# Kernel tuning notes

Hardware: AMD Instinct MI355X
Metric: run time of the kernel (lower is better)

## Reference

```python
import jax, jax.numpy as jnp
import numpy as np
import math

NH, NKV, D = 32, 8, 128  # heads, kv heads, head dim

def _alibi_slopes(n):
    cp2 = 2 ** math.floor(math.log2(n))
    base = 2.0 ** (-8.0 / cp2)
    slopes = base ** np.arange(1, cp2 + 1, dtype=np.float32)
    if cp2 != n:
        extra_base = 2.0 ** (-4.0 / cp2)
        extra = extra_base ** np.arange(1, 1 + 2 * (n - cp2), 2, dtype=np.float32)
        slopes = np.concatenate([slopes, extra])
    return slopes.astype(np.float32)

def setup_inputs() -> dict:
    key = jax.random.key(0)
    k1, k2, k3 = jax.random.split(key, 3)
    B, S, H = 4, 1024, 4096
    qkv_out = NH * D + 2 * NKV * D  # 6144
    return {
        "hidden_states": jax.random.normal(k1, (B, S, H), jnp.float32) * 0.02,
        "w_qkv": jax.random.normal(k2, (H, qkv_out), jnp.float32) * 0.02,
        "w_o": jax.random.normal(k3, (NH * D, H), jnp.float32) * 0.02,
    }

def reference(hidden_states, w_qkv, w_o):
    B, S, H = hidden_states.shape
    G = NH // NKV  # query groups per kv head
    scale = D ** -0.5

    qkv = hidden_states @ w_qkv  # [B,S,6144]
    q = qkv[..., : NH * D].reshape(B, S, NKV, G, D)
    k = qkv[..., NH * D : NH * D + NKV * D].reshape(B, S, NKV, D)
    v = qkv[..., NH * D + NKV * D :].reshape(B, S, NKV, D)

    scores = jnp.einsum("bqhgd,bkhd->bhgqk", q, k) * scale  # [B,NKV,G,S,S]

    slopes = jnp.asarray(_alibi_slopes(NH)).reshape(NKV, G)  # head order
    pos = jnp.arange(S)
    rel = pos[:, None] - pos[None, :]  # i - j
    sqrt_dist = jnp.sqrt(jnp.maximum(rel, 0).astype(jnp.float32))
    bias = -slopes[:, :, None, None] * sqrt_dist  # ALiBi-sqrt bias
    bias = jnp.where(rel[None, None] >= 0, bias, -jnp.inf)  # causal mask

    attn = jax.nn.softmax(scores + bias[None], axis=-1)
    out = jnp.einsum("bhgqk,bkhd->bqhgd", attn, v).reshape(B, S, NH * D)
    return out @ w_o
```

## Files before the change

kernel.cpp:

```cpp
#include <hip/hip_runtime.h>
#include <stdint.h>

typedef __attribute__((ext_vector_type(4))) float floatx4;
typedef __attribute__((ext_vector_type(8))) short short8;
typedef unsigned short ushort_t;

#define DEVI __device__ __forceinline__

constexpr int Bc   = 4;
constexpr int Sc   = 1024;
constexpr int Hc   = 4096;
constexpr int NHc  = 32;
constexpr int NKVc = 8;
constexpr int Dc   = 128;
constexpr int QKVO = 6144;
constexpr int Mc   = Bc * Sc;

DEVI ushort_t f2bf(float f) {
  union { float f; unsigned u; } x; x.f = f;
  unsigned u = x.u;
  u += 0x7fffu + ((u >> 16) & 1u);
  return (ushort_t)(u >> 16);
}

DEVI short8 cvt8(floatx4 a, floatx4 b) {
  short8 r;
  r[0] = (short)f2bf(a[0]); r[1] = (short)f2bf(a[1]);
  r[2] = (short)f2bf(a[2]); r[3] = (short)f2bf(a[3]);
  r[4] = (short)f2bf(b[0]); r[5] = (short)f2bf(b[1]);
  r[6] = (short)f2bf(b[2]); r[7] = (short)f2bf(b[3]);
  return r;
}

DEVI void load_lds16(const ushort_t* g, ushort_t* l) {
  __builtin_amdgcn_global_load_lds(
      (const __attribute__((address_space(1))) void*)g,
      (__attribute__((address_space(3))) void*)l, 16, 0, 0);
}

#define BARRIER()  asm volatile("s_barrier" ::: "memory")
#define VMCNT(n)   asm volatile("s_waitcnt vmcnt(" #n ")" ::: "memory")

__global__ __launch_bounds__(256)
void cvt_bf16(const float* __restrict__ src, ushort_t* __restrict__ dst, int n8)
{
  const int i = blockIdx.x * 256 + threadIdx.x;
  if (i >= n8) return;
  const floatx4 f0 = *(const floatx4*)(src + (size_t)i * 8);
  const floatx4 f1 = *(const floatx4*)(src + (size_t)i * 8 + 4);
  *(short8*)(dst + (size_t)i * 8) = cvt8(f0, f1);
}

__global__ __launch_bounds__(256)
void transpose_cvt(const float* __restrict__ src, ushort_t* __restrict__ dst,
                   int R, int C)
{
  __shared__ float ts[64][67];
  const int cb = C >> 6;
  const int r0 = (blockIdx.x / cb) << 6;
  const int c0 = (blockIdx.x % cb) << 6;
  const int t  = threadIdx.x;

  const int lr = t >> 4, lc = (t & 15) << 2;
#pragma unroll
  for (int i = 0; i < 4; ++i) {
    const floatx4 v = *(const floatx4*)(src + (size_t)(r0 + lr + 16 * i) * C + c0 + lc);
#pragma unroll
    for (int j = 0; j < 4; ++j) ts[lr + 16 * i][lc + j] = v[j];
  }
  __syncthreads();

  const int c     = ((t >> 6) << 4) + ((t & 63) >> 2);
  const int chunk = t & 3;
  short8 t0, t1;
#pragma unroll
  for (int k = 0; k < 8; ++k) t0[k] = (short)f2bf(ts[chunk * 16 + k][c]);
#pragma unroll
  for (int k = 0; k < 8; ++k) t1[k] = (short)f2bf(ts[chunk * 16 + 8 + k][c]);
  ushort_t* dp = dst + (size_t)(c0 + c) * R + r0 + chunk * 16;
  *(short8*)dp       = t0;
  *(short8*)(dp + 8) = t1;
}

__global__ __launch_bounds__(256)
void v_transpose(const ushort_t* __restrict__ qkv, ushort_t* __restrict__ vt)
{
  __shared__ ushort_t ts[64][72];
  const int bid = blockIdx.x;
  const int db  = bid & 1;
  const int sb  = (bid >> 1) & 15;
  const int hkv = (bid >> 5) & 7;
  const int b   = bid >> 8;
  const int t   = threadIdx.x;

  const ushort_t* src = qkv + (size_t)(b * Sc + sb * 64) * QKVO
                        + (NHc * Dc + NKVc * Dc) + hkv * Dc + db * 64;
  const int lr = t >> 3, lc = (t & 7) * 8;
  *(short8*)&ts[lr][lc]      = *(const short8*)(src + (size_t)lr * QKVO + lc);
  *(short8*)&ts[lr + 32][lc] = *(const short8*)(src + (size_t)(lr + 32) * QKVO + lc);
  __syncthreads();

  ushort_t* dst = vt + ((size_t)(b * NKVc + hkv) * Dc + db * 64) * Sc + sb * 64;
  const int dr  = t >> 2;
  const int sc0 = (t & 3) * 16;
  short8 o0, o1;
#pragma unroll
  for (int k = 0; k < 8; ++k) o0[k] = (short)ts[sc0 + k][dr];
#pragma unroll
  for (int k = 0; k < 8; ++k) o1[k] = (short)ts[sc0 + 8 + k][dr];
  *(short8*)(dst + (size_t)dr * Sc + sc0)     = o0;
  *(short8*)(dst + (size_t)dr * Sc + sc0 + 8) = o1;
}

template<bool OBF16>
__global__ __launch_bounds__(512, 2)
void gemm_nt8(const ushort_t* __restrict__ A, const ushort_t* __restrict__ BT,
              void* __restrict__ Cp, int M, int N, int K)
{
  __shared__ __align__(16) ushort_t As[2][256 * 64];
  __shared__ __align__(16) ushort_t Bs[2][256 * 64];

  const int nb  = N >> 8;
  const int nwg = (M >> 8) * nb;
  int bid = blockIdx.x;
  bid = (bid & 7) * (nwg >> 3) + (bid >> 3);
  const int bm = bid / nb, bn = bid % nb;
  const int m0 = bm << 8, n0 = bn << 8;

  const int tid  = threadIdx.x;
  const int wid  = tid >> 6, lane = tid & 63;
  const int wm   = wid >> 2, wn = wid & 3;
  const int fr   = lane & 15;
  const int g16  = (lane >> 4) << 4;
  const int rsw  = (fr & 7) << 4;
  const int l8   = lane >> 3;
  const int scol = ((lane & 7) ^ l8) << 3;

  const int abase = ((wid >> 2) << 7) + ((wid & 3) << 4);
  const int bbase = wid << 5;

  const size_t Ks = (size_t)K;
  const ushort_t* ag = A  + (size_t)(m0 + abase + l8) * K + scol;
  const ushort_t* bg = BT + (size_t)(n0 + bbase + l8) * K + scol;

  const int rowA = (wm * 128 + fr) * 128;
  const int rowB = (wn * 64 + fr) * 128;
  const int cb0  = g16 ^ rsw;
  const int cb1  = (64 + g16) ^ rsw;

  const floatx4 fz = {0.f, 0.f, 0.f, 0.f};
  floatx4 acc[8][4];
#pragma unroll
  for (int i = 0; i < 8; ++i)
#pragma unroll
    for (int f = 0; f < 4; ++f) acc[i][f] = fz;

  auto STAGE = [&](int v, size_t kn) {
    load_lds16(ag + kn,            &As[v][(abase +  0) * 64]);
    load_lds16(ag +  8 * Ks + kn,  &As[v][(abase +  8) * 64]);
    load_lds16(bg + kn,            &Bs[v][(bbase +  0) * 64]);
    load_lds16(bg +  8 * Ks + kn,  &Bs[v][(bbase +  8) * 64]);
    load_lds16(ag + 64 * Ks + kn,  &As[v][(abase + 64) * 64]);
    load_lds16(ag + 72 * Ks + kn,  &As[v][(abase + 72) * 64]);
    load_lds16(bg + 16 * Ks + kn,  &Bs[v][(bbase + 16) * 64]);
    load_lds16(bg + 24 * Ks + kn,  &Bs[v][(bbase + 24) * 64]);
  };

  STAGE(0, 0);
  VMCNT(4);
  BARRIER();

  const int NT = K >> 6;
  for (int kt = 0; kt < NT; ++kt) {
    const int u = kt & 1, v = u ^ 1;
    const char* Au = (const char*)&As[u][0];
    const char* Bu = (const char*)&Bs[u][0];
    const bool st  = (kt + 1 < NT);

#define LDA(i, ks) (*(const short8*)(Au + rowA + (i) * 2048 + ((ks) ? cb1 : cb0)))
#define LDB(f, ks) (*(const short8*)(Bu + rowB + (f) * 2048 + ((ks) ? cb1 : cb0)))
#define MFMA16(d, a0, a1, b0, b1)                                         \
    d = __builtin_amdgcn_mfma_f32_16x16x32_bf16(a0, b0, d, 0, 0, 0);      \
    d = __builtin_amdgcn_mfma_f32_16x16x32_bf16(a1, b1, d, 0, 0, 0);

    short8 aL[4][2], aH[4][2], bE[2][2], bO[2][2];

#pragma unroll
    for (int i = 0; i < 4; ++i) { aL[i][0] = LDA(i, 0); aL[i][1] = LDA(i, 1); }
#pragma unroll
    for (int f = 0; f < 2; ++f) { bE[f][0] = LDB(2 * f, 0); bE[f][1] = LDB(2 * f, 1); }
    if (st) STAGE(v, (size_t)(kt + 1) << 6);
    BARRIER();
    __builtin_amdgcn_s_setprio(1);
#pragma unroll
    for (int i = 0; i < 4; ++i)
#pragma unroll
      for (int f = 0; f < 2; ++f) { MFMA16(acc[i][2 * f], aL[i][0], aL[i][1], bE[f][0], bE[f][1]); }
    __builtin_amdgcn_s_setprio(0);
    if (st) { VMCNT(10); } else { VMCNT(2); }
    BARRIER();

#pragma unroll
    for (int i = 0; i < 4; ++i) { aH[i][0] = LDA(4 + i, 0); aH[i][1] = LDA(4 + i, 1); }
    BARRIER();
    __builtin_amdgcn_s_setprio(1);
#pragma unroll
    for (int i = 0; i < 4; ++i)
#pragma unroll
      for (int f = 0; f < 2; ++f) { MFMA16(acc[4 + i][2 * f], aH[i][0], aH[i][1], bE[f][0], bE[f][1]); }
    __builtin_amdgcn_s_setprio(0);
    if (st) { VMCNT(8); } else { VMCNT(0); }
    BARRIER();

#pragma unroll
    for (int f = 0; f < 2; ++f) { bO[f][0] = LDB(2 * f + 1, 0); bO[f][1] = LDB(2 * f + 1, 1); }
    BARRIER();
    __builtin_amdgcn_s_setprio(1);
#pragma unroll
    for (int i = 0; i < 4; ++i)
#pragma unroll
      for (int f = 0; f < 2; ++f) { MFMA16(acc[4 + i][2 * f + 1], aH[i][0], aH[i][1], bO[f][0], bO[f][1]); }
    __builtin_amdgcn_s_setprio(0);
    BARRIER();

    __builtin_amdgcn_s_setprio(1);
#pragma unroll
    for (int i = 0; i < 4; ++i)
#pragma unroll
      for (int f = 0; f < 2; ++f) { MFMA16(acc[i][2 * f + 1], aL[i][0], aL[i][1], bO[f][0], bO[f][1]); }
    __builtin_amdgcn_s_setprio(0);
    if (st) { VMCNT(4); }
    BARRIER();

#undef LDA
#undef LDB
#undef MFMA16
  }

  const int r4 = (lane >> 4) << 2;
#pragma unroll
  for (int i = 0; i < 8; ++i) {
#pragma unroll
    for (int rr = 0; rr < 4; ++rr) {
      const size_t row = (size_t)(m0 + wm * 128 + i * 16 + r4 + rr);
#pragma unroll
      for (int f = 0; f < 4; ++f) {
        const size_t col = (size_t)(n0 + wn * 64 + f * 16 + fr);
        if constexpr (OBF16)
          ((ushort_t*)Cp)[row * N + col] = f2bf(acc[i][f][rr]);
        else
          ((float*)Cp)[row * N + col] = acc[i][f][rr];
      }
    }
  }
}

__global__ __launch_bounds__(256, 2)
void attn_fwd(const ushort_t* __restrict__ qkv,
              const ushort_t* __restrict__ vt,
              ushort_t* __restrict__ attn)
{
  __shared__ __align__(16) ushort_t Plds[4][32 * 40];

  const int bid = blockIdx.x;
  const int x   = bid & 7;
  const int p   = bid >> 3;
  const int j   = p & 15;
  const int g   = ((p >> 4) << 3) + x;
  const int b   = g >> 3;
  const int hkv = g & 7;

  const int tid  = threadIdx.x;
  const int wid  = tid >> 6, lane = tid & 63;
  const int h    = hkv * 4 + wid;
  const int fr   = lane & 15;
  const int kk8  = (lane >> 4) << 3;
  const int q4   = (lane >> 4) << 2;
  const float slope = exp2f(-0.25f * (float)(h + 1));
  const float scale = 0.08838834764831845f;

  const ushort_t* qp  = qkv + (size_t)b * Sc * QKVO + (size_t)h * Dc;
  const ushort_t* kp  = qkv + (size_t)b * Sc * QKVO + NHc * Dc + (size_t)hkv * Dc;
  const ushort_t* vtp = vt + (size_t)(b * NKVc + hkv) * Dc * Sc;
  ushort_t* myP = &Plds[wid][0];

  const floatx4 fz = {0.f, 0.f, 0.f, 0.f};

  auto process = [&](const int qb) {
    short8 qf[2][4];
#pragma unroll
    for (int t = 0; t < 2; ++t) {
      const int qrow = qb * 32 + t * 16 + fr;
#pragma unroll
      for (int s = 0; s < 4; ++s)
        qf[t][s] = *(const short8*)(qp + (size_t)qrow * QKVO + s * 32 + kk8);
    }

    floatx4 o[2][8];
#pragma unroll
    for (int t = 0; t < 2; ++t)
#pragma unroll
      for (int jj = 0; jj < 8; ++jj) o[t][jj] = fz;
    float mrow[2][4], lrow[2][4];
#pragma unroll
    for (int t = 0; t < 2; ++t)
#pragma unroll
      for (int rr = 0; rr < 4; ++rr) { mrow[t][rr] = -1e30f; lrow[t][rr] = 0.f; }

    for (int kb = 0; kb <= qb; ++kb) {
      floatx4 s_[2][2];
      s_[0][0] = fz; s_[0][1] = fz; s_[1][0] = fz; s_[1][1] = fz;
#pragma unroll
      for (int half = 0; half < 2; ++half) {
        const int kcol = kb * 32 + half * 16 + fr;
#pragma unroll
        for (int s = 0; s < 4; ++s) {
          const short8 kf = *(const short8*)(kp + (size_t)kcol * QKVO + s * 32 + kk8);
          s_[0][half] = __builtin_amdgcn_mfma_f32_16x16x32_bf16(qf[0][s], kf, s_[0][half], 0, 0, 0);
          s_[1][half] = __builtin_amdgcn_mfma_f32_16x16x32_bf16(qf[1][s], kf, s_[1][half], 0, 0, 0);
        }
      }

      short8 vf[8];
#pragma unroll
      for (int jj = 0; jj < 8; ++jj)
        vf[jj] = *(const short8*)(vtp + (size_t)(jj * 16 + fr) * Sc + kb * 32 + kk8);

#pragma unroll
      for (int t = 0; t < 2; ++t)
#pragma unroll
        for (int rr = 0; rr < 4; ++rr) {
          const int qg  = qb * 32 + t * 16 + q4 + rr;
          const int dk0 = qg - (kb * 32 + fr);
          const int dk1 = dk0 - 16;
          s_[t][0][rr] = (dk0 >= 0)
              ? s_[t][0][rr] * scale - slope * sqrtf((float)dk0) : -1e30f;
          s_[t][1][rr] = (dk1 >= 0)
              ? s_[t][1][rr] * scale - slope * sqrtf((float)dk1) : -1e30f;
        }

      float pmv[2][4];
#pragma unroll
      for (int t = 0; t < 2; ++t)
#pragma unroll
        for (int rr = 0; rr < 4; ++rr) {
          float pm = fmaxf(s_[t][0][rr], s_[t][1][rr]);
#pragma unroll
          for (int m = 1; m < 16; m <<= 1) pm = fmaxf(pm, __shfl_xor(pm, m));
          pmv[t][rr] = pm;
        }

      int need = 0;
#pragma unroll
      for (int t = 0; t < 2; ++t)
#pragma unroll
        for (int rr = 0; rr < 4; ++rr)
          need |= (pmv[t][rr] > mrow[t][rr] + 8.f) ? 1 : 0;
      if (__any(need)) {
#pragma unroll
        for (int t = 0; t < 2; ++t)
#pragma unroll
          for (int rr = 0; rr < 4; ++rr) {
            const float mnew = fmaxf(mrow[t][rr], pmv[t][rr]);
            const float corr = __expf(mrow[t][rr] - mnew);
            lrow[t][rr] *= corr;
            mrow[t][rr] = mnew;
#pragma unroll
            for (int jj = 0; jj < 8; ++jj) o[t][jj][rr] *= corr;
          }
      }

#pragma unroll
      for (int t = 0; t < 2; ++t)
#pragma unroll
        for (int rr = 0; rr < 4; ++rr) {
          const float p0 = __expf(s_[t][0][rr] - mrow[t][rr]);
          const float p1 = __expf(s_[t][1][rr] - mrow[t][rr]);
          lrow[t][rr] += p0 + p1;
          myP[(t * 16 + q4 + rr) * 40 + fr]      = f2bf(p0);
          myP[(t * 16 + q4 + rr) * 40 + 16 + fr] = f2bf(p1);
        }
      short8 pa[2];
      pa[0] = *(const short8*)&myP[fr * 40 + kk8];
      pa[1] = *(const short8*)&myP[(16 + fr) * 40 + kk8];

#pragma unroll
      for (int jj = 0; jj < 8; ++jj) {
        o[0][jj] = __builtin_amdgcn_mfma_f32_16x16x32_bf16(pa[0], vf[jj], o[0][jj], 0, 0, 0);
        o[1][jj] = __builtin_amdgcn_mfma_f32_16x16x32_bf16(pa[1], vf[jj], o[1][jj], 0, 0, 0);
      }
    }

#pragma unroll
    for (int t = 0; t < 2; ++t)
#pragma unroll
      for (int rr = 0; rr < 4; ++rr) {
        float rs = lrow[t][rr];
#pragma unroll
        for (int m = 1; m < 16; m <<= 1) rs += __shfl_xor(rs, m);
        const float inv = 1.f / rs;
        const size_t tok = (size_t)b * Sc + qb * 32 + t * 16 + q4 + rr;
#pragma unroll
        for (int jj = 0; jj < 8; ++jj)
          attn[tok * (size_t)(NHc * Dc) + h * Dc + jj * 16 + fr] = f2bf(o[t][jj][rr] * inv);
      }
  };

  process(31 - j);
  process(j);
}

extern "C" void kernel_launch(void* const* d_in, const int* in_sizes, int n_in,
                              void* d_out, int out_size, void* d_ws, size_t ws_size,
                              hipStream_t stream)
{
  const float* hidden = (const float*)d_in[0];
  const float* w_qkv  = (const float*)d_in[1];
  const float* w_o    = (const float*)d_in[2];
  float* out = (float*)d_out;

  ushort_t* wqT   = (ushort_t*)d_ws;
  ushort_t* hidb  = wqT + (size_t)QKVO * Hc;
  ushort_t* qkvb  = hidb + (size_t)Mc * Hc;
  ushort_t* attnb = hidb;
  ushort_t* woT   = wqT;
  ushort_t* vtb   = wqT + (size_t)Mc * Hc;

  cvt_bf16<<<dim3((Mc * Hc / 8) / 256), dim3(256), 0, stream>>>(
      hidden, hidb, Mc * Hc / 8);
  transpose_cvt<<<dim3((Hc / 64) * (QKVO / 64)), dim3(256), 0, stream>>>(
      w_qkv, wqT, Hc, QKVO);
  gemm_nt8<true><<<dim3((Mc / 256) * (QKVO / 256)), dim3(512), 0, stream>>>(
      hidb, wqT, qkvb, Mc, QKVO, Hc);
  v_transpose<<<dim3(1024), dim3(256), 0, stream>>>(qkvb, vtb);
  attn_fwd<<<dim3(512), dim3(256), 0, stream>>>(qkvb, vtb, attnb);
  transpose_cvt<<<dim3((Hc / 64) * (Hc / 64)), dim3(256), 0, stream>>>(
      w_o, woT, Hc, Hc);
  gemm_nt8<false><<<dim3((Mc / 256) * (Hc / 256)), dim3(512), 0, stream>>>(
      attnb, woT, out, Mc, Hc, Hc);
}
```

Before: 578.9 us.

## Restructure GEMM main loop into K-half phases with split A/B staging

Result: slower. 599.1 us (+3.5%).

```diff
diff --git a/kernel.cpp b/kernel.cpp
--- a/kernel.cpp
+++ b/kernel.cpp
@@ -39,6 +39,7 @@
 }
 
 #define BARRIER()  asm volatile("s_barrier" ::: "memory")
+#define LGKM0()    asm volatile("s_waitcnt lgkmcnt(0)" ::: "memory")
 #define VMCNT(n)   asm volatile("s_waitcnt vmcnt(" #n ")" ::: "memory")
 
 __global__ __launch_bounds__(256)
@@ -136,12 +137,10 @@
   const int l8   = lane >> 3;
   const int scol = ((lane & 7) ^ l8) << 3;
 
-  const int abase = ((wid >> 2) << 7) + ((wid & 3) << 4);
-  const int bbase = wid << 5;
-
+  const int sr   = (wid << 3);
   const size_t Ks = (size_t)K;
-  const ushort_t* ag = A  + (size_t)(m0 + abase + l8) * K + scol;
-  const ushort_t* bg = BT + (size_t)(n0 + bbase + l8) * K + scol;
+  const ushort_t* agS = A  + (size_t)(m0 + sr + l8) * K + scol;
+  const ushort_t* bgS = BT + (size_t)(n0 + sr + l8) * K + scol;
 
   const int rowA = (wm * 128 + fr) * 128;
   const int rowB = (wn * 64 + fr) * 128;
@@ -155,19 +154,21 @@
 #pragma unroll
     for (int f = 0; f < 4; ++f) acc[i][f] = fz;
 
-  auto STAGE = [&](int v, size_t kn) {
-    load_lds16(ag + kn,            &As[v][(abase +  0) * 64]);
-    load_lds16(ag +  8 * Ks + kn,  &As[v][(abase +  8) * 64]);
-    load_lds16(bg + kn,            &Bs[v][(bbase +  0) * 64]);
-    load_lds16(bg +  8 * Ks + kn,  &Bs[v][(bbase +  8) * 64]);
-    load_lds16(ag + 64 * Ks + kn,  &As[v][(abase + 64) * 64]);
-    load_lds16(ag + 72 * Ks + kn,  &As[v][(abase + 72) * 64]);
-    load_lds16(bg + 16 * Ks + kn,  &Bs[v][(bbase + 16) * 64]);
-    load_lds16(bg + 24 * Ks + kn,  &Bs[v][(bbase + 24) * 64]);
+  auto STB = [&](int v, size_t kn) {
+    load_lds16(bgS + kn,            &Bs[v][(sr +   0) * 64]);
+    load_lds16(bgS +  64 * Ks + kn, &Bs[v][(sr +  64) * 64]);
+    load_lds16(bgS + 128 * Ks + kn, &Bs[v][(sr + 128) * 64]);
+    load_lds16(bgS + 192 * Ks + kn, &Bs[v][(sr + 192) * 64]);
   };
-
-  STAGE(0, 0);
-  VMCNT(4);
+  auto STA = [&](int v, size_t kn) {
+    load_lds16(agS + kn,            &As[v][(sr +   0) * 64]);
+    load_lds16(agS + 128 * Ks + kn, &As[v][(sr + 128) * 64]);
+    load_lds16(agS +  64 * Ks + kn, &As[v][(sr +  64) * 64]);
+    load_lds16(agS + 192 * Ks + kn, &As[v][(sr + 192) * 64]);
+  };
+
+  STB(0, 0); STA(0, 0);
+  VMCNT(2);
   BARRIER();
 
   const int NT = K >> 6;
@@ -176,65 +177,74 @@
     const char* Au = (const char*)&As[u][0];
     const char* Bu = (const char*)&Bs[u][0];
     const bool st  = (kt + 1 < NT);
+    const size_t kn = (size_t)(kt + 1) << 6;
 
 #define LDA(i, ks) (*(const short8*)(Au + rowA + (i) * 2048 + ((ks) ? cb1 : cb0)))
 #define LDB(f, ks) (*(const short8*)(Bu + rowB + (f) * 2048 + ((ks) ? cb1 : cb0)))
-#define MFMA16(d, a0, a1, b0, b1)                                         \
-    d = __builtin_amdgcn_mfma_f32_16x16x32_bf16(a0, b0, d, 0, 0, 0);      \
-    d = __builtin_amdgcn_mfma_f32_16x16x32_bf16(a1, b1, d, 0, 0, 0);
-
-    short8 aL[4][2], aH[4][2], bE[2][2], bO[2][2];
-
-#pragma unroll
-    for (int i = 0; i < 4; ++i) { aL[i][0] = LDA(i, 0); aL[i][1] = LDA(i, 1); }
-#pragma unroll
-    for (int f = 0; f < 2; ++f) { bE[f][0] = LDB(2 * f, 0); bE[f][1] = LDB(2 * f, 1); }
-    if (st) STAGE(v, (size_t)(kt + 1) << 6);
-    BARRIER();
+
+    short8 aR[4], bR[4];
+
+#pragma unroll
+    for (int i = 0; i < 4; ++i) aR[i] = LDA(i, 0);
+#pragma unroll
+    for (int f = 0; f < 4; ++f) bR[f] = LDB(f, 0);
+    if (st) { STB(v, kn); VMCNT(4); } else { VMCNT(0); }
+    BARRIER();
+    LGKM0(); __builtin_amdgcn_sched_barrier(0);
     __builtin_amdgcn_s_setprio(1);
 #pragma unroll
     for (int i = 0; i < 4; ++i)
 #pragma unroll
-      for (int f = 0; f < 2; ++f) { MFMA16(acc[i][2 * f], aL[i][0], aL[i][1], bE[f][0], bE[f][1]); }
+      for (int f = 0; f < 4; ++f)
+        acc[i][f] = __builtin_amdgcn_mfma_f32_16x16x32_bf16(aR[i], bR[f], acc[i][f], 0, 0, 0);
     __builtin_amdgcn_s_setprio(0);
-    if (st) { VMCNT(10); } else { VMCNT(2); }
-    BARRIER();
-
-#pragma unroll
-    for (int i = 0; i < 4; ++i) { aH[i][0] = LDA(4 + i, 0); aH[i][1] = LDA(4 + i, 1); }
-    BARRIER();
+    BARRIER();
+
+#pragma unroll
+    for (int i = 0; i < 4; ++i) aR[i] = LDA(4 + i, 0);
+    if (st) STA(v, kn);
+    BARRIER();
+    LGKM0(); __builtin_amdgcn_sched_barrier(0);
     __builtin_amdgcn_s_setprio(1);
 #pragma unroll
     for (int i = 0; i < 4; ++i)
 #pragma unroll
-      for (int f = 0; f < 2; ++f) { MFMA16(acc[4 + i][2 * f], aH[i][0], aH[i][1], bE[f][0], bE[f][1]); }
+      for (int f = 0; f < 4; ++f)
+        acc[4 + i][f] = __builtin_amdgcn_mfma_f32_16x16x32_bf16(aR[i], bR[f], acc[4 + i][f], 0, 0, 0);
     __builtin_amdgcn_s_setprio(0);
-    if (st) { VMCNT(8); } else { VMCNT(0); }
-    BARRIER();
-
-#pragma unroll
-    for (int f = 0; f < 2; ++f) { bO[f][0] = LDB(2 * f + 1, 0); bO[f][1] = LDB(2 * f + 1, 1); }
-    BARRIER();
+    BARRIER();
+
+#pragma unroll
+    for (int i = 0; i < 4; ++i) aR[i] = LDA(4 + i, 1);
+#pragma unroll
+    for (int f = 0; f < 4; ++f) bR[f] = LDB(f, 1);
+    BARRIER();
+    LGKM0(); __builtin_amdgcn_sched_barrier(0);
     __builtin_amdgcn_s_setprio(1);
 #pragma unroll
     for (int i = 0; i < 4; ++i)
 #pragma unroll
-      for (int f = 0; f < 2; ++f) { MFMA16(acc[4 + i][2 * f + 1], aH[i][0], aH[i][1], bO[f][0], bO[f][1]); }
+      for (int f = 0; f < 4; ++f)
+        acc[4 + i][f] = __builtin_amdgcn_mfma_f32_16x16x32_bf16(aR[i], bR[f], acc[4 + i][f], 0, 0, 0);
     __builtin_amdgcn_s_setprio(0);
     BARRIER();
 
+#pragma unroll
+    for (int i = 0; i < 4; ++i) aR[i] = LDA(i, 1);
+    if (st) { VMCNT(2); }
+    BARRIER();
+    LGKM0(); __builtin_amdgcn_sched_barrier(0);
     __builtin_amdgcn_s_setprio(1);
 #pragma unroll
     for (int i = 0; i < 4; ++i)
 #pragma unroll
-      for (int f = 0; f < 2; ++f) { MFMA16(acc[i][2 * f + 1], aL[i][0], aL[i][1], bO[f][0], bO[f][1]); }
+      for (int f = 0; f < 4; ++f)
+        acc[i][f] = __builtin_amdgcn_mfma_f32_16x16x32_bf16(aR[i], bR[f], acc[i][f], 0, 0, 0);
     __builtin_amdgcn_s_setprio(0);
-    if (st) { VMCNT(4); }
     BARRIER();
 
 #undef LDA
 #undef LDB
-#undef MFMA16
   }
 
   const int r4 = (lane >> 4) << 2;
```
